# Kernel tuning notes

Hardware: AMD Instinct MI355X
Metric: run time of the kernel (lower is better)

Reference implementation:

```python
import jax, jax.numpy as jnp
import numpy as np

B, SQ, ST, SI = 8, 4096, 77, 16
C, DC, H = 1280, 2048, 20
DH = C // H  # 64
SCALE = 1.0 / np.sqrt(DH).astype(np.float32)
SCALE_ID = 1.0
SCALE_HAIR = 1.0


def setup_inputs() -> dict:
    key = jax.random.key(0)
    ks = jax.random.split(key, 12)
    std = 0.02
    return {
        "hidden_states": jax.random.normal(ks[0], (B, SQ, C), jnp.float32),
        "text_states": jax.random.normal(ks[1], (B, ST, DC), jnp.float32),
        "id_states": jax.random.normal(ks[2], (B, SI, DC), jnp.float32),
        "hair_states": jax.random.normal(ks[3], (B, SI, DC), jnp.float32),
        # weights stored as [in, out] (transpose of torch nn.Linear layout)
        "Wq": jax.random.normal(ks[4], (C, C), jnp.float32) * std,
        "Wk": jax.random.normal(ks[5], (DC, C), jnp.float32) * std,
        "Wv": jax.random.normal(ks[6], (DC, C), jnp.float32) * std,
        "Wo": jax.random.normal(ks[7], (C, C), jnp.float32) * std,
        "b_o": jnp.zeros((C,), jnp.float32),
        "Wk_id": jax.random.normal(ks[8], (DC, C), jnp.float32) * std,
        "Wv_id": jax.random.normal(ks[9], (DC, C), jnp.float32) * std,
        "Wk_hair": jax.random.normal(ks[10], (DC, C), jnp.float32) * std,
        "Wv_hair": jax.random.normal(ks[11], (DC, C), jnp.float32) * std,
    }


def _heads(x):
    # [B, S, C] -> [B, H, S, DH]
    b, s, _ = x.shape
    return x.reshape(b, s, H, DH).transpose(0, 2, 1, 3)


def _merge(x):
    # [B, H, S, DH] -> [B, S, C]
    b, h, s, d = x.shape
    return x.transpose(0, 2, 1, 3).reshape(b, s, h * d)


def _attend(q, k, v):
    # q: [B,H,Sq,DH], k/v: [B,H,Sk,DH]; fp32 scores (attn_fp32=True)
    scores = jnp.einsum("bhqd,bhkd->bhqk", q.astype(jnp.float32), k.astype(jnp.float32)) * SCALE
    p = jax.nn.softmax(scores, axis=-1)
    return jnp.einsum("bhqk,bhkd->bhqd", p, v.astype(jnp.float32))


def reference(hidden_states, text_states, id_states, hair_states, Wq, Wk, Wv, Wo, b_o, Wk_id, Wv_id, Wk_hair, Wv_hair):
    q = _heads(hidden_states @ Wq)
    # base cross-attention to text (standard diffusers AttnProcessor)
    base = _attend(q, _heads(text_states @ Wk), _heads(text_states @ Wv))
    result = _merge(base) @ Wo + b_o
    # ID branch: own K/V projections, shared query and to_out
    out_id = _attend(q, _heads(id_states @ Wk_id), _heads(id_states @ Wv_id))
    result = result + SCALE_ID * (_merge(out_id) @ Wo + b_o)
    # hair branch
    out_h = _attend(q, _heads(hair_states @ Wk_hair), _heads(hair_states @ Wv_hair))
    result = result + SCALE_HAIR * (_merge(out_h) @ Wo + b_o)
    return result
```

## Files before the change

kernel.cpp:

```cpp
#include <hip/hip_runtime.h>
#include <cstdint>
#include <cstddef>

typedef unsigned short u16;
typedef __attribute__((ext_vector_type(4))) float     f32x4_t;
typedef __attribute__((ext_vector_type(8))) __bf16    bf16x8_t;
typedef __attribute__((ext_vector_type(8))) u16       u16x8_t;
typedef __attribute__((ext_vector_type(4))) u16       u16x4_t;
typedef __attribute__((ext_vector_type(4))) float     fvec4_t;

#define DEVI __device__ __forceinline__

constexpr int Bn  = 8;
constexpr int SQn = 4096;
constexpr int STn = 77;
constexpr int SIn = 16;
constexpr int Cn  = 1280;
constexpr int DCn = 2048;
constexpr int Hn  = 20;
constexpr float SCALEf = 0.125f;
constexpr float L2E    = 1.4426950408889634f;

typedef const __attribute__((address_space(1))) void* gas_t;
typedef __attribute__((address_space(3))) void*       las_t;

DEVI u16 f2bf(float f) {
  union { float f; unsigned u; } cv; cv.f = f;
  unsigned u = cv.u;
  return (u16)((u + 0x7FFFu + ((u >> 16) & 1u)) >> 16);
}

__global__ __launch_bounds__(256) void cast_bf16_kernel(
    const float* __restrict__ src, u16* __restrict__ dst, int n8) {
  int i = blockIdx.x * 256 + threadIdx.x;
  if (i >= n8) return;
  const fvec4_t* s4 = (const fvec4_t*)src;
  fvec4_t a = s4[2 * i], b = s4[2 * i + 1];
  u16x8_t o;
  o[0] = f2bf(a[0]); o[1] = f2bf(a[1]); o[2] = f2bf(a[2]); o[3] = f2bf(a[3]);
  o[4] = f2bf(b[0]); o[5] = f2bf(b[1]); o[6] = f2bf(b[2]); o[7] = f2bf(b[3]);
  ((u16x8_t*)dst)[i] = o;
}

struct TrArgs {
  const float* src[8];
  u16*         dst[8];
  int          Kd[8];
};

__global__ __launch_bounds__(256) void transpose_cast_kernel(TrArgs ta) {
  int z = blockIdx.z;
  int K = ta.Kd[z];
  int k0 = blockIdx.x * 32;
  if (k0 >= K) return;
  int n0 = blockIdx.y * 32;
  __shared__ float tile[32][33];
  int tx = threadIdx.x & 31, ty = threadIdx.x >> 5;
  const float* src = ta.src[z];
#pragma unroll
  for (int i = 0; i < 4; i++) {
    int r = ty + 8 * i;
    tile[r][tx] = src[(size_t)(k0 + r) * Cn + n0 + tx];
  }
  __syncthreads();
  u16* dst = ta.dst[z];
#pragma unroll
  for (int i = 0; i < 4; i++) {
    int r = ty + 8 * i;
    dst[(size_t)(n0 + r) * K + k0 + tx] = f2bf(tile[tx][r]);
  }
}

template <int OUT_MODE, int A_HM>
__global__ __launch_bounds__(512, 2) void gemm256_kernel(
    const u16* __restrict__ A, const u16* __restrict__ Bt,
    void* __restrict__ Cout, const float* __restrict__ bias, int M, int K) {
  __shared__ __align__(16) u16 lds[2][2][256 * 64];
  const int t = threadIdx.x;
  const int w = t >> 6, l = t & 63;
  const int wr = w >> 2, wc = w & 3;
  const int lr = l & 15;
  const int m0 = blockIdx.x * 256, n0 = blockIdx.y * 256;
  const int NT = K >> 6;

  f32x4_t acc[8][4];
#pragma unroll
  for (int am = 0; am < 8; am++)
#pragma unroll
    for (int an = 0; an < 4; an++) {
      f32x4_t z = {0.f, 0.f, 0.f, 0.f};
      acc[am][an] = z;
    }

  auto stagePart = [&](int cb, int kt, int i) {
    const int k0 = kt * 64;
    int row = i * 64 + w * 8 + (l >> 3);
    int col16 = (l & 7) ^ (row & 7);
    const u16* ga;
    if (A_HM) {
      int gr = m0 + row, bb = gr >> 12, ss = gr & 4095;
      ga = A + (((size_t)bb * Hn + kt) * SQn + ss) * 64 + col16 * 8;
    } else {
      ga = A + (size_t)(m0 + row) * K + k0 + col16 * 8;
    }
    __builtin_amdgcn_global_load_lds((gas_t)ga, (las_t)(&lds[cb][0][0] + (size_t)(i * 512 + w * 64) * 8), 16, 0, 0);
    const u16* gb = Bt + (size_t)(n0 + row) * K + k0 + col16 * 8;
    __builtin_amdgcn_global_load_lds((gas_t)gb, (las_t)(&lds[cb][1][0] + (size_t)(i * 512 + w * 64) * 8), 16, 0, 0);
  };
  auto readA8 = [&](bf16x8_t (&dst)[8], const u16* bA, int kh) {
#pragma unroll
    for (int m = 0; m < 8; m++) {
      int row = wr * 128 + m * 16 + lr;
      int slot = kh * 4 + (l >> 4);
      dst[m] = *(const bf16x8_t*)&bA[row * 64 + ((slot ^ (row & 7)) * 8)];
    }
  };
  auto readB4 = [&](bf16x8_t (&dst)[4], const u16* bB, int kh) {
#pragma unroll
    for (int n = 0; n < 4; n++) {
      int row = wc * 64 + n * 16 + lr;
      int slot = kh * 4 + (l >> 4);
      dst[n] = *(const bf16x8_t*)&bB[row * 64 + ((slot ^ (row & 7)) * 8)];
    }
  };
  auto mfma32 = [&](bf16x8_t (&Af)[8], bf16x8_t (&Bf)[4]) {
    __builtin_amdgcn_s_setprio(1);
#pragma unroll
    for (int m = 0; m < 8; m++)
#pragma unroll
      for (int n = 0; n < 4; n++)
        acc[m][n] = __builtin_amdgcn_mfma_f32_16x16x32_bf16(Af[m], Bf[n], acc[m][n], 0, 0, 0);
    __builtin_amdgcn_s_setprio(0);
  };

#pragma unroll
  for (int i = 0; i < 4; i++) stagePart(0, 0, i);
#pragma unroll
  for (int i = 0; i < 4; i++) stagePart(1, 1, i);
  asm volatile("s_waitcnt vmcnt(8)" ::: "memory");
  __builtin_amdgcn_sched_barrier(0);
  __builtin_amdgcn_s_barrier();

  for (int kt = 0; kt < NT; kt++) {
    const int cb = kt & 1;
    const u16* bA = &lds[cb][0][0];
    const u16* bB = &lds[cb][1][0];
    const bool st = (kt + 2 < NT);
    bf16x8_t Af[8], Bf[4];

    readA8(Af, bA, 0);
    readB4(Bf, bB, 0);
    asm volatile("s_waitcnt lgkmcnt(0)" ::: "memory");
    __builtin_amdgcn_sched_barrier(0);
    mfma32(Af, Bf);

    readA8(Af, bA, 1);
    readB4(Bf, bB, 1);
    __builtin_amdgcn_s_barrier();
    if (st) {
      stagePart(cb, kt + 2, 0); stagePart(cb, kt + 2, 1);
      stagePart(cb, kt + 2, 2); stagePart(cb, kt + 2, 3);
    }
    asm volatile("s_waitcnt lgkmcnt(0)" ::: "memory");
    __builtin_amdgcn_sched_barrier(0);
    mfma32(Af, Bf);

    if (st) {
      asm volatile("s_waitcnt vmcnt(8)" ::: "memory");
    } else if (kt + 1 < NT) {
      asm volatile("s_waitcnt vmcnt(0)" ::: "memory");
    }
    __builtin_amdgcn_sched_barrier(0);
    __builtin_amdgcn_s_barrier();
  }

#pragma unroll
  for (int am = 0; am < 8; am++) {
    int rbase = m0 + wr * 128 + am * 16 + (l >> 4) * 4;
#pragma unroll
    for (int an = 0; an < 4; an++) {
      int col = n0 + wc * 64 + an * 16 + lr;
#pragma unroll
      for (int j = 0; j < 4; j++) {
        int r = rbase + j;
        if (OUT_MODE == 1) {
          ((float*)Cout)[(size_t)r * Cn + col] = acc[am][an][j] + 3.0f * bias[col];
        } else {
          int bb = r >> 12, ss = r & 4095;
          int hh = (n0 >> 6) + wc, dd = an * 16 + lr;
          ((u16*)Cout)[(((size_t)bb * Hn + hh) * SQn + ss) * 64 + dd] = f2bf(acc[am][an][j]);
        }
      }
    }
  }
}

DEVI void gemm_body(const u16* __restrict__ A, const u16* __restrict__ Bt,
                    u16* __restrict__ Cout, int M, int S, int K, int mtile, int ntile) {
  __shared__ __align__(16) u16 lA[128 * 64];
  __shared__ __align__(16) u16 lB[128 * 64];
  const int t = threadIdx.x;
  const int w = t >> 6, l = t & 63;
  const int wr = w >> 1, wc = w & 1;
  const int m0 = mtile * 128, n0 = ntile * 128;
  const int lr = l & 15, lk = (l >> 4) * 8;

  f32x4_t acc[4][4];
#pragma unroll
  for (int m = 0; m < 4; m++)
#pragma unroll
    for (int n = 0; n < 4; n++) {
      f32x4_t z = {0.f, 0.f, 0.f, 0.f};
      acc[m][n] = z;
    }

  for (int k0 = 0; k0 < K; k0 += 64) {
    __syncthreads();
#pragma unroll
    for (int i = 0; i < 4; i++) {
      int c = i * 256 + t;
      int row = c >> 3, ch = c & 7;
      int rA = m0 + row;
      rA = rA < M ? rA : M - 1;
      const u16* ga = A + (size_t)rA * K + k0 + ch * 8;
      __builtin_amdgcn_global_load_lds((gas_t)ga, (las_t)&lA[(i * 256 + w * 64) * 8], 16, 0, 0);
      const u16* gb = Bt + (size_t)(n0 + row) * K + k0 + ch * 8;
      __builtin_amdgcn_global_load_lds((gas_t)gb, (las_t)&lB[(i * 256 + w * 64) * 8], 16, 0, 0);
    }
    __syncthreads();
#pragma unroll
    for (int kk = 0; kk < 2; kk++) {
      bf16x8_t af[4], bf[4];
#pragma unroll
      for (int m = 0; m < 4; m++)
        af[m] = *(const bf16x8_t*)&lA[(64 * wr + 16 * m + lr) * 64 + kk * 32 + lk];
#pragma unroll
      for (int n = 0; n < 4; n++)
        bf[n] = *(const bf16x8_t*)&lB[(64 * wc + 16 * n + lr) * 64 + kk * 32 + lk];
#pragma unroll
      for (int m = 0; m < 4; m++)
#pragma unroll
        for (int n = 0; n < 4; n++)
          acc[m][n] = __builtin_amdgcn_mfma_f32_16x16x32_bf16(af[m], bf[n], acc[m][n], 0, 0, 0);
    }
  }

  const int rj = (l >> 4) * 4;
  const int hh = ntile * 2 + wc;
#pragma unroll
  for (int m = 0; m < 4; m++) {
    int rbase = m0 + 64 * wr + 16 * m + rj;
#pragma unroll
    for (int n = 0; n < 4; n++) {
      int dd = 16 * n + lr;
#pragma unroll
      for (int j = 0; j < 4; j++) {
        int r = rbase + j;
        if (r < M) {
          int bb = r / S, ss = r - bb * S;
          Cout[(((size_t)bb * Hn + hh) * S + ss) * 64 + dd] = f2bf(acc[m][n][j]);
        }
      }
    }
  }
}

struct KV6 {
  const u16* A[6];
  const u16* Bt[6];
  u16*       Cp[6];
  int        M[6];
  int        S[6];
};

__global__ __launch_bounds__(256) void gemm_kv_kernel(KV6 kv) {
  int z = blockIdx.z;
  int M = kv.M[z];
  if ((int)blockIdx.x * 128 >= M) return;
  gemm_body(kv.A[z], kv.Bt[z], kv.Cp[z], M, kv.S[z], DCn, blockIdx.x, blockIdx.y);
}

__global__ __launch_bounds__(256) void attn_kernel(
    const u16* __restrict__ q,
    const u16* __restrict__ ktx, const u16* __restrict__ vtx,
    const u16* __restrict__ kid, const u16* __restrict__ vid,
    const u16* __restrict__ kh,  const u16* __restrict__ vh,
    u16* __restrict__ osum) {
  __shared__ __align__(16) u16 KP[4 * 16 * 136];
  __shared__ __align__(16) u16 Vt[64 * 128];

  const int t = threadIdx.x, w = t >> 6, l = t & 63;
  const int bh = blockIdx.y;
  const int lr = l & 15, lk = (l >> 4) * 8;

  const u16* qB   = q   + ((size_t)bh) * SQn * 64;
  const u16* ktxB = ktx + ((size_t)bh) * STn * 64;
  const u16* vtxB = vtx + ((size_t)bh) * STn * 64;
  const u16* kidB = kid + ((size_t)bh) * SIn * 64;
  const u16* vidB = vid + ((size_t)bh) * SIn * 64;
  const u16* khB  = kh  + ((size_t)bh) * SIn * 64;
  const u16* vhB  = vh  + ((size_t)bh) * SIn * 64;
  u16*       oB   = osum + ((size_t)bh) * SQn * 64;

  for (int i = t; i < 112 * 8; i += 256) {
    int row = i >> 3, ch = i & 7;
    u16x8_t vv;
#pragma unroll
    for (int x = 0; x < 8; x++) vv[x] = 0;
    if (row < 77)
      vv = *(const u16x8_t*)(ktxB + (size_t)row * 64 + ch * 8);
    else if (row >= 80 && row < 96)
      vv = *(const u16x8_t*)(kidB + (size_t)(row - 80) * 64 + ch * 8);
    else if (row >= 96)
      vv = *(const u16x8_t*)(khB + (size_t)(row - 96) * 64 + ch * 8);
    *(u16x8_t*)&KP[row * 72 + ch * 8] = vv;
  }
  for (int i = t; i < 128 * 8; i += 256) {
    int key = i >> 3, ch = i & 7;
    u16x8_t vv;
#pragma unroll
    for (int x = 0; x < 8; x++) vv[x] = 0;
    if (key < 77)
      vv = *(const u16x8_t*)(vtxB + (size_t)key * 64 + ch * 8);
    else if (key >= 80 && key < 96)
      vv = *(const u16x8_t*)(vidB + (size_t)(key - 80) * 64 + ch * 8);
    else if (key >= 96 && key < 112)
      vv = *(const u16x8_t*)(vhB + (size_t)(key - 96) * 64 + ch * 8);
    int G = key >> 3, wk = key & 7;
#pragma unroll
    for (int x = 0; x < 8; x++) {
      int d = ch * 8 + x;
      int Gs = G ^ x ^ ch;
      Vt[d * 128 + Gs * 8 + wk] = vv[x];
    }
  }
  __syncthreads();

  bf16x8_t kf[7][2];
#pragma unroll
  for (int tt = 0; tt < 7; tt++)
#pragma unroll
    for (int kk = 0; kk < 2; kk++)
      kf[tt][kk] = *(const bf16x8_t*)&KP[(tt * 16 + lr) * 72 + kk * 32 + lk];
  __syncthreads();

  u16* Pw = &KP[w * 16 * 136];
  {
    u16x4_t z4; z4[0] = 0; z4[1] = 0; z4[2] = 0; z4[3] = 0;
    *(u16x4_t*)&Pw[(l >> 2) * 136 + 112 + (l & 3) * 4] = z4;
  }

  for (int rt = 0; rt < 8; rt++) {
    const int s0 = blockIdx.x * 512 + w * 128 + rt * 16;
    bf16x8_t qf[2];
#pragma unroll
    for (int kk = 0; kk < 2; kk++)
      qf[kk] = *(const bf16x8_t*)&qB[(size_t)(s0 + lr) * 64 + kk * 32 + lk];

    f32x4_t sc[7];
#pragma unroll
    for (int tt = 0; tt < 7; tt++) {
      f32x4_t z = {0.f, 0.f, 0.f, 0.f};
      z = __builtin_amdgcn_mfma_f32_16x16x32_bf16(qf[0], kf[tt][0], z, 0, 0, 0);
      z = __builtin_amdgcn_mfma_f32_16x16x32_bf16(qf[1], kf[tt][1], z, 0, 0, 0);
      sc[tt] = z;
    }
#pragma unroll
    for (int tt = 0; tt < 7; tt++)
#pragma unroll
      for (int j = 0; j < 4; j++) sc[tt][j] *= SCALEf;
    if (lr >= 13) {
#pragma unroll
      for (int j = 0; j < 4; j++) sc[4][j] = -3.0e38f;
    }

    float mx[4], sm[4], inv[4];

#pragma unroll
    for (int j = 0; j < 4; j++) {
      float m = sc[0][j];
      m = fmaxf(m, sc[1][j]); m = fmaxf(m, sc[2][j]);
      m = fmaxf(m, sc[3][j]); m = fmaxf(m, sc[4][j]);
      mx[j] = m;
    }
#pragma unroll
    for (int d = 1; d < 16; d <<= 1)
#pragma unroll
      for (int j = 0; j < 4; j++) mx[j] = fmaxf(mx[j], __shfl_xor(mx[j], d));
#pragma unroll
    for (int j = 0; j < 4; j++) sm[j] = 0.f;
#pragma unroll
    for (int tt = 0; tt < 5; tt++)
#pragma unroll
      for (int j = 0; j < 4; j++) {
        float p = __builtin_amdgcn_exp2f((sc[tt][j] - mx[j]) * L2E);
        sc[tt][j] = p;
        sm[j] += p;
      }
#pragma unroll
    for (int d = 1; d < 16; d <<= 1)
#pragma unroll
      for (int j = 0; j < 4; j++) sm[j] += __shfl_xor(sm[j], d);
#pragma unroll
    for (int j = 0; j < 4; j++) inv[j] = __builtin_amdgcn_rcpf(sm[j]);
#pragma unroll
    for (int tt = 0; tt < 5; tt++)
#pragma unroll
      for (int j = 0; j < 4; j++) {
        __bf16 pb = (__bf16)(sc[tt][j] * inv[j]);
        Pw[((l >> 4) * 4 + j) * 136 + tt * 16 + lr] = *(u16*)&pb;
      }

#pragma unroll
    for (int j = 0; j < 4; j++) mx[j] = sc[5][j];
#pragma unroll
    for (int d = 1; d < 16; d <<= 1)
#pragma unroll
      for (int j = 0; j < 4; j++) mx[j] = fmaxf(mx[j], __shfl_xor(mx[j], d));
#pragma unroll
    for (int j = 0; j < 4; j++) {
      float p = __builtin_amdgcn_exp2f((sc[5][j] - mx[j]) * L2E);
      sc[5][j] = p;
      sm[j] = p;
    }
#pragma unroll
    for (int d = 1; d < 16; d <<= 1)
#pragma unroll
      for (int j = 0; j < 4; j++) sm[j] += __shfl_xor(sm[j], d);
#pragma unroll
    for (int j = 0; j < 4; j++) {
      __bf16 pb = (__bf16)(sc[5][j] * __builtin_amdgcn_rcpf(sm[j]));
      Pw[((l >> 4) * 4 + j) * 136 + 80 + lr] = *(u16*)&pb;
    }

#pragma unroll
    for (int j = 0; j < 4; j++) mx[j] = sc[6][j];
#pragma unroll
    for (int d = 1; d < 16; d <<= 1)
#pragma unroll
      for (int j = 0; j < 4; j++) mx[j] = fmaxf(mx[j], __shfl_xor(mx[j], d));
#pragma unroll
    for (int j = 0; j < 4; j++) {
      float p = __builtin_amdgcn_exp2f((sc[6][j] - mx[j]) * L2E);
      sc[6][j] = p;
      sm[j] = p;
    }
#pragma unroll
    for (int d = 1; d < 16; d <<= 1)
#pragma unroll
      for (int j = 0; j < 4; j++) sm[j] += __shfl_xor(sm[j], d);
#pragma unroll
    for (int j = 0; j < 4; j++) {
      __bf16 pb = (__bf16)(sc[6][j] * __builtin_amdgcn_rcpf(sm[j]));
      Pw[((l >> 4) * 4 + j) * 136 + 96 + lr] = *(u16*)&pb;
    }

    f32x4_t oacc[4];
#pragma unroll
    for (int n = 0; n < 4; n++) {
      f32x4_t z = {0.f, 0.f, 0.f, 0.f};
      oacc[n] = z;
    }
#pragma unroll
    for (int ktile = 0; ktile < 4; ktile++) {
      bf16x8_t pf = *(const bf16x8_t*)&Pw[lr * 136 + ktile * 32 + lk];
#pragma unroll
      for (int n = 0; n < 4; n++) {
        int d = 16 * n + lr;
        int Gs = (4 * ktile + (l >> 4)) ^ (d & 7) ^ ((d >> 3) & 7);
        bf16x8_t vf = *(const bf16x8_t*)&Vt[d * 128 + Gs * 8];
        oacc[n] = __builtin_amdgcn_mfma_f32_16x16x32_bf16(pf, vf, oacc[n], 0, 0, 0);
      }
    }
#pragma unroll
    for (int n = 0; n < 4; n++)
#pragma unroll
      for (int j = 0; j < 4; j++) {
        int srow = s0 + (l >> 4) * 4 + j;
        __bf16 ob = (__bf16)oacc[n][j];
        oB[(size_t)srow * 64 + 16 * n + lr] = *(u16*)&ob;
      }
  }
}

extern "C" void kernel_launch(void* const* d_in, const int* in_sizes, int n_in,
                              void* d_out, int out_size, void* d_ws, size_t ws_size,
                              hipStream_t stream) {
  (void)in_sizes; (void)n_in; (void)out_size; (void)ws_size;
  const float* hidden  = (const float*)d_in[0];
  const float* text    = (const float*)d_in[1];
  const float* ids     = (const float*)d_in[2];
  const float* hair    = (const float*)d_in[3];
  const float* Wq      = (const float*)d_in[4];
  const float* Wk      = (const float*)d_in[5];
  const float* Wv      = (const float*)d_in[6];
  const float* Wo      = (const float*)d_in[7];
  const float* b_o     = (const float*)d_in[8];
  const float* Wk_id   = (const float*)d_in[9];
  const float* Wv_id   = (const float*)d_in[10];
  const float* Wk_hair = (const float*)d_in[11];
  const float* Wv_hair = (const float*)d_in[12];
  float* out = (float*)d_out;

  char* ws = (char*)d_ws;
  size_t off = 0;
  auto carve = [&](size_t bytes) -> char* {
    char* p = ws + off;
    off += (bytes + 255) & ~(size_t)255;
    return p;
  };

  u16* h_bf    = (u16*)carve((size_t)Bn * SQn * Cn * 2);
  u16* q_bf    = (u16*)carve((size_t)Bn * SQn * Cn * 2);
  u16* text_bf = (u16*)carve((size_t)Bn * STn * DCn * 2);
  u16* id_bf   = (u16*)carve((size_t)Bn * SIn * DCn * 2);
  u16* hair_bf = (u16*)carve((size_t)Bn * SIn * DCn * 2);
  u16* Wq_t    = (u16*)carve((size_t)Cn * Cn * 2);
  u16* Wo_t    = (u16*)carve((size_t)Cn * Cn * 2);
  u16* Wk_t    = (u16*)carve((size_t)DCn * Cn * 2);
  u16* Wv_t    = (u16*)carve((size_t)DCn * Cn * 2);
  u16* Wkid_t  = (u16*)carve((size_t)DCn * Cn * 2);
  u16* Wvid_t  = (u16*)carve((size_t)DCn * Cn * 2);
  u16* Wkh_t   = (u16*)carve((size_t)DCn * Cn * 2);
  u16* Wvh_t   = (u16*)carve((size_t)DCn * Cn * 2);
  u16* k_text  = (u16*)carve((size_t)Bn * STn * Cn * 2);
  u16* v_text  = (u16*)carve((size_t)Bn * STn * Cn * 2);
  u16* k_id    = (u16*)carve((size_t)Bn * SIn * Cn * 2);
  u16* v_id    = (u16*)carve((size_t)Bn * SIn * Cn * 2);
  u16* k_hr    = (u16*)carve((size_t)Bn * SIn * Cn * 2);
  u16* v_hr    = (u16*)carve((size_t)Bn * SIn * Cn * 2);
  u16* attn_sum = h_bf;

  {
    int n8 = Bn * SQn * Cn / 8;
    cast_bf16_kernel<<<dim3((n8 + 255) / 256), 256, 0, stream>>>(hidden, h_bf, n8);
  }
  {
    int n8 = Bn * STn * DCn / 8;
    cast_bf16_kernel<<<dim3((n8 + 255) / 256), 256, 0, stream>>>(text, text_bf, n8);
  }
  {
    int n8 = Bn * SIn * DCn / 8;
    cast_bf16_kernel<<<dim3((n8 + 255) / 256), 256, 0, stream>>>(ids, id_bf, n8);
    cast_bf16_kernel<<<dim3((n8 + 255) / 256), 256, 0, stream>>>(hair, hair_bf, n8);
  }

  {
    TrArgs ta;
    ta.src[0] = Wq;      ta.dst[0] = Wq_t;   ta.Kd[0] = Cn;
    ta.src[1] = Wo;      ta.dst[1] = Wo_t;   ta.Kd[1] = Cn;
    ta.src[2] = Wk;      ta.dst[2] = Wk_t;   ta.Kd[2] = DCn;
    ta.src[3] = Wv;      ta.dst[3] = Wv_t;   ta.Kd[3] = DCn;
    ta.src[4] = Wk_id;   ta.dst[4] = Wkid_t; ta.Kd[4] = DCn;
    ta.src[5] = Wv_id;   ta.dst[5] = Wvid_t; ta.Kd[5] = DCn;
    ta.src[6] = Wk_hair; ta.dst[6] = Wkh_t;  ta.Kd[6] = DCn;
    ta.src[7] = Wv_hair; ta.dst[7] = Wvh_t;  ta.Kd[7] = DCn;
    transpose_cast_kernel<<<dim3(DCn / 32, Cn / 32, 8), 256, 0, stream>>>(ta);
  }

  gemm256_kernel<2, 0><<<dim3(Bn * SQn / 256, Cn / 256), 512, 0, stream>>>(
      h_bf, Wq_t, q_bf, nullptr, Bn * SQn, Cn);

  {
    KV6 kv;
    kv.A[0] = text_bf; kv.Bt[0] = Wk_t;   kv.Cp[0] = k_text; kv.M[0] = Bn * STn; kv.S[0] = STn;
    kv.A[1] = text_bf; kv.Bt[1] = Wv_t;   kv.Cp[1] = v_text; kv.M[1] = Bn * STn; kv.S[1] = STn;
    kv.A[2] = id_bf;   kv.Bt[2] = Wkid_t; kv.Cp[2] = k_id;   kv.M[2] = Bn * SIn; kv.S[2] = SIn;
    kv.A[3] = id_bf;   kv.Bt[3] = Wvid_t; kv.Cp[3] = v_id;   kv.M[3] = Bn * SIn; kv.S[3] = SIn;
    kv.A[4] = hair_bf; kv.Bt[4] = Wkh_t;  kv.Cp[4] = k_hr;   kv.M[4] = Bn * SIn; kv.S[4] = SIn;
    kv.A[5] = hair_bf; kv.Bt[5] = Wvh_t;  kv.Cp[5] = v_hr;   kv.M[5] = Bn * SIn; kv.S[5] = SIn;
    gemm_kv_kernel<<<dim3((Bn * STn + 127) / 128, Cn / 128, 6), 256, 0, stream>>>(kv);
  }

  attn_kernel<<<dim3(SQn / 512, Bn * Hn), 256, 0, stream>>>(
      q_bf, k_text, v_text, k_id, v_id, k_hr, v_hr, attn_sum);

  gemm256_kernel<1, 1><<<dim3(Bn * SQn / 256, Cn / 256), 512, 0, stream>>>(
      attn_sum, Wo_t, out, b_o, Bn * SQn, Cn);
}
```

Baseline: 475.5 us.

## Merge input casts into one launch and co-schedule Q and KV projections

The four separate fp32-to-bf16 cast launches become one kernel that picks its source and destination from the flat thread index. The Q projection GEMM and the six small K/V projection GEMMs now share a single launch: the first 640 blocks compute 256x256 Q tiles, and the remaining 70 blocks each run two 128x128 K/V tiles, one per 256-thread half. This removes launch gaps and lets the small K/V work fill the tail of the Q GEMM. The cost is a shared 128KB LDS allocation for the K/V blocks, and both halves of a block must keep their barriers in lockstep, which holds because they run the same K loop.

```diff
diff --git a/kernel.cpp b/kernel.cpp
--- a/kernel.cpp
+++ b/kernel.cpp
@@ -21,6 +21,12 @@
 constexpr float SCALEf = 0.125f;
 constexpr float L2E    = 1.4426950408889634f;
 
+constexpr int CAST_N0 = Bn * SQn * Cn / 8;
+constexpr int CAST_N1 = Bn * STn * DCn / 8;
+constexpr int CAST_N2 = Bn * SIn * DCn / 8;
+constexpr int CAST_N3 = Bn * SIn * DCn / 8;
+constexpr int CAST_NT = CAST_N0 + CAST_N1 + CAST_N2 + CAST_N3;
+
 typedef const __attribute__((address_space(1))) void* gas_t;
 typedef __attribute__((address_space(3))) void*       las_t;
 
@@ -30,16 +36,23 @@
   return (u16)((u + 0x7FFFu + ((u >> 16) & 1u)) >> 16);
 }
 
-__global__ __launch_bounds__(256) void cast_bf16_kernel(
-    const float* __restrict__ src, u16* __restrict__ dst, int n8) {
+__global__ __launch_bounds__(256) void cast4_kernel(
+    const float* __restrict__ hs, const float* __restrict__ tx,
+    const float* __restrict__ idp, const float* __restrict__ hrp,
+    u16* __restrict__ dh, u16* __restrict__ dt,
+    u16* __restrict__ di, u16* __restrict__ dr) {
   int i = blockIdx.x * 256 + threadIdx.x;
-  if (i >= n8) return;
+  const float* src; u16* dst; int off;
+  if (i < CAST_N0)                              { src = hs;  dst = dh; off = i; }
+  else if (i < CAST_N0 + CAST_N1)               { src = tx;  dst = dt; off = i - CAST_N0; }
+  else if (i < CAST_N0 + CAST_N1 + CAST_N2)     { src = idp; dst = di; off = i - CAST_N0 - CAST_N1; }
+  else                                          { src = hrp; dst = dr; off = i - CAST_N0 - CAST_N1 - CAST_N2; }
   const fvec4_t* s4 = (const fvec4_t*)src;
-  fvec4_t a = s4[2 * i], b = s4[2 * i + 1];
+  fvec4_t a = s4[2 * off], b = s4[2 * off + 1];
   u16x8_t o;
   o[0] = f2bf(a[0]); o[1] = f2bf(a[1]); o[2] = f2bf(a[2]); o[3] = f2bf(a[3]);
   o[4] = f2bf(b[0]); o[5] = f2bf(b[1]); o[6] = f2bf(b[2]); o[7] = f2bf(b[3]);
-  ((u16x8_t*)dst)[i] = o;
+  ((u16x8_t*)dst)[off] = o;
 }
 
 struct TrArgs {
@@ -72,15 +85,15 @@
 }
 
 template <int OUT_MODE, int A_HM>
-__global__ __launch_bounds__(512, 2) void gemm256_kernel(
-    const u16* __restrict__ A, const u16* __restrict__ Bt,
-    void* __restrict__ Cout, const float* __restrict__ bias, int M, int K) {
-  __shared__ __align__(16) u16 lds[2][2][256 * 64];
+DEVI void gemm256_body(u16* sm, const u16* __restrict__ A,
+                       const u16* __restrict__ Bt, void* __restrict__ Cout,
+                       const float* __restrict__ bias, int M, int K,
+                       int mtile, int ntile) {
   const int t = threadIdx.x;
   const int w = t >> 6, l = t & 63;
   const int wr = w >> 2, wc = w & 3;
   const int lr = l & 15;
-  const int m0 = blockIdx.x * 256, n0 = blockIdx.y * 256;
+  const int m0 = mtile * 256, n0 = ntile * 256;
   const int NT = K >> 6;
 
   f32x4_t acc[8][4];
@@ -103,9 +116,9 @@
     } else {
       ga = A + (size_t)(m0 + row) * K + k0 + col16 * 8;
     }
-    __builtin_amdgcn_global_load_lds((gas_t)ga, (las_t)(&lds[cb][0][0] + (size_t)(i * 512 + w * 64) * 8), 16, 0, 0);
+    __builtin_amdgcn_global_load_lds((gas_t)ga, (las_t)(sm + (size_t)(cb * 2 + 0) * 16384 + (size_t)(i * 512 + w * 64) * 8), 16, 0, 0);
     const u16* gb = Bt + (size_t)(n0 + row) * K + k0 + col16 * 8;
-    __builtin_amdgcn_global_load_lds((gas_t)gb, (las_t)(&lds[cb][1][0] + (size_t)(i * 512 + w * 64) * 8), 16, 0, 0);
+    __builtin_amdgcn_global_load_lds((gas_t)gb, (las_t)(sm + (size_t)(cb * 2 + 1) * 16384 + (size_t)(i * 512 + w * 64) * 8), 16, 0, 0);
   };
   auto readA8 = [&](bf16x8_t (&dst)[8], const u16* bA, int kh) {
 #pragma unroll
@@ -143,8 +156,8 @@
 
   for (int kt = 0; kt < NT; kt++) {
     const int cb = kt & 1;
-    const u16* bA = &lds[cb][0][0];
-    const u16* bB = &lds[cb][1][0];
+    const u16* bA = sm + (size_t)(cb * 2 + 0) * 16384;
+    const u16* bB = sm + (size_t)(cb * 2 + 1) * 16384;
     const bool st = (kt + 2 < NT);
     bf16x8_t Af[8], Bf[4];
 
@@ -195,12 +208,12 @@
   }
 }
 
-DEVI void gemm_body(const u16* __restrict__ A, const u16* __restrict__ Bt,
-                    u16* __restrict__ Cout, int M, int S, int K, int mtile, int ntile) {
-  __shared__ __align__(16) u16 lA[128 * 64];
-  __shared__ __align__(16) u16 lB[128 * 64];
-  const int t = threadIdx.x;
-  const int w = t >> 6, l = t & 63;
+DEVI void kv_body(u16* lsA, int th, const u16* __restrict__ A,
+                  const u16* __restrict__ Bt, u16* __restrict__ Cout,
+                  int M, int S, int mtile, int ntile) {
+  u16* lA = lsA;
+  u16* lB = lsA + 8192;
+  const int w = th >> 6, l = th & 63;
   const int wr = w >> 1, wc = w & 1;
   const int m0 = mtile * 128, n0 = ntile * 128;
   const int lr = l & 15, lk = (l >> 4) * 8;
@@ -214,17 +227,17 @@
       acc[m][n] = z;
     }
 
-  for (int k0 = 0; k0 < K; k0 += 64) {
+  for (int k0 = 0; k0 < DCn; k0 += 64) {
     __syncthreads();
 #pragma unroll
     for (int i = 0; i < 4; i++) {
-      int c = i * 256 + t;
+      int c = i * 256 + th;
       int row = c >> 3, ch = c & 7;
       int rA = m0 + row;
       rA = rA < M ? rA : M - 1;
-      const u16* ga = A + (size_t)rA * K + k0 + ch * 8;
+      const u16* ga = A + (size_t)rA * DCn + k0 + ch * 8;
       __builtin_amdgcn_global_load_lds((gas_t)ga, (las_t)&lA[(i * 256 + w * 64) * 8], 16, 0, 0);
-      const u16* gb = Bt + (size_t)(n0 + row) * K + k0 + ch * 8;
+      const u16* gb = Bt + (size_t)(n0 + row) * DCn + k0 + ch * 8;
       __builtin_amdgcn_global_load_lds((gas_t)gb, (las_t)&lB[(i * 256 + w * 64) * 8], 16, 0, 0);
     }
     __syncthreads();
@@ -265,19 +278,34 @@
   }
 }
 
-struct KV6 {
-  const u16* A[6];
-  const u16* Bt[6];
-  u16*       Cp[6];
-  int        M[6];
-  int        S[6];
+struct QKVArgs {
+  const u16* hq;  const u16* WqT;  u16* qout;
+  const u16* A[6]; const u16* Bt[6]; u16* Cp[6]; int M[6]; int S[6];
 };
 
-__global__ __launch_bounds__(256) void gemm_kv_kernel(KV6 kv) {
-  int z = blockIdx.z;
-  int M = kv.M[z];
-  if ((int)blockIdx.x * 128 >= M) return;
-  gemm_body(kv.A[z], kv.Bt[z], kv.Cp[z], M, kv.S[z], DCn, blockIdx.x, blockIdx.y);
+__global__ __launch_bounds__(512, 2) void gemm_q_kv_kernel(QKVArgs a) {
+  __shared__ __align__(16) u16 sm[65536];
+  const int bx = blockIdx.x;
+  if (bx < 640) {
+    gemm256_body<2, 0>(sm, a.hq, a.WqT, a.qout, nullptr,
+                       Bn * SQn, Cn, bx % 128, bx / 128);
+  } else {
+    const int p = bx - 640;
+    const int h = threadIdx.x >> 8;
+    const int kt = p * 2 + h;
+    int z, mt, nt;
+    if (kt < 100) { z = kt / 50; int r = kt % 50; mt = r / 10; nt = r % 10; }
+    else          { int r = kt - 100; z = 2 + r / 10; mt = 0; nt = r % 10; }
+    kv_body(sm + (size_t)h * 16384, threadIdx.x & 255,
+            a.A[z], a.Bt[z], a.Cp[z], a.M[z], a.S[z], mt, nt);
+  }
+}
+
+__global__ __launch_bounds__(512, 2) void gemm_o_kernel(
+    const u16* __restrict__ A, const u16* __restrict__ Bt,
+    float* __restrict__ Cout, const float* __restrict__ bias, int M, int K) {
+  __shared__ __align__(16) u16 sm[65536];
+  gemm256_body<1, 1>(sm, A, Bt, Cout, bias, M, K, blockIdx.x, blockIdx.y);
 }
 
 __global__ __launch_bounds__(256) void attn_kernel(
@@ -531,19 +559,8 @@
   u16* v_hr    = (u16*)carve((size_t)Bn * SIn * Cn * 2);
   u16* attn_sum = h_bf;
 
-  {
-    int n8 = Bn * SQn * Cn / 8;
-    cast_bf16_kernel<<<dim3((n8 + 255) / 256), 256, 0, stream>>>(hidden, h_bf, n8);
-  }
-  {
-    int n8 = Bn * STn * DCn / 8;
-    cast_bf16_kernel<<<dim3((n8 + 255) / 256), 256, 0, stream>>>(text, text_bf, n8);
-  }
-  {
-    int n8 = Bn * SIn * DCn / 8;
-    cast_bf16_kernel<<<dim3((n8 + 255) / 256), 256, 0, stream>>>(ids, id_bf, n8);
-    cast_bf16_kernel<<<dim3((n8 + 255) / 256), 256, 0, stream>>>(hair, hair_bf, n8);
-  }
+  cast4_kernel<<<dim3(CAST_NT / 256), 256, 0, stream>>>(
+      hidden, text, ids, hair, h_bf, text_bf, id_bf, hair_bf);
 
   {
     TrArgs ta;
@@ -558,23 +575,21 @@
     transpose_cast_kernel<<<dim3(DCn / 32, Cn / 32, 8), 256, 0, stream>>>(ta);
   }
 
-  gemm256_kernel<2, 0><<<dim3(Bn * SQn / 256, Cn / 256), 512, 0, stream>>>(
-      h_bf, Wq_t, q_bf, nullptr, Bn * SQn, Cn);
-
   {
-    KV6 kv;
-    kv.A[0] = text_bf; kv.Bt[0] = Wk_t;   kv.Cp[0] = k_text; kv.M[0] = Bn * STn; kv.S[0] = STn;
-    kv.A[1] = text_bf; kv.Bt[1] = Wv_t;   kv.Cp[1] = v_text; kv.M[1] = Bn * STn; kv.S[1] = STn;
-    kv.A[2] = id_bf;   kv.Bt[2] = Wkid_t; kv.Cp[2] = k_id;   kv.M[2] = Bn * SIn; kv.S[2] = SIn;
-    kv.A[3] = id_bf;   kv.Bt[3] = Wvid_t; kv.Cp[3] = v_id;   kv.M[3] = Bn * SIn; kv.S[3] = SIn;
-    kv.A[4] = hair_bf; kv.Bt[4] = Wkh_t;  kv.Cp[4] = k_hr;   kv.M[4] = Bn * SIn; kv.S[4] = SIn;
-    kv.A[5] = hair_bf; kv.Bt[5] = Wvh_t;  kv.Cp[5] = v_hr;   kv.M[5] = Bn * SIn; kv.S[5] = SIn;
-    gemm_kv_kernel<<<dim3((Bn * STn + 127) / 128, Cn / 128, 6), 256, 0, stream>>>(kv);
+    QKVArgs a;
+    a.hq = h_bf; a.WqT = Wq_t; a.qout = q_bf;
+    a.A[0] = text_bf; a.Bt[0] = Wk_t;   a.Cp[0] = k_text; a.M[0] = Bn * STn; a.S[0] = STn;
+    a.A[1] = text_bf; a.Bt[1] = Wv_t;   a.Cp[1] = v_text; a.M[1] = Bn * STn; a.S[1] = STn;
+    a.A[2] = id_bf;   a.Bt[2] = Wkid_t; a.Cp[2] = k_id;   a.M[2] = Bn * SIn; a.S[2] = SIn;
+    a.A[3] = id_bf;   a.Bt[3] = Wvid_t; a.Cp[3] = v_id;   a.M[3] = Bn * SIn; a.S[3] = SIn;
+    a.A[4] = hair_bf; a.Bt[4] = Wkh_t;  a.Cp[4] = k_hr;   a.M[4] = Bn * SIn; a.S[4] = SIn;
+    a.A[5] = hair_bf; a.Bt[5] = Wvh_t;  a.Cp[5] = v_hr;   a.M[5] = Bn * SIn; a.S[5] = SIn;
+    gemm_q_kv_kernel<<<dim3(710), 512, 0, stream>>>(a);
   }
 
   attn_kernel<<<dim3(SQn / 512, Bn * Hn), 256, 0, stream>>>(
       q_bf, k_text, v_text, k_id, v_id, k_hr, v_hr, attn_sum);
 
-  gemm256_kernel<1, 1><<<dim3(Bn * SQn / 256, Cn / 256), 512, 0, stream>>>(
+  gemm_o_kernel<<<dim3(Bn * SQn / 256, Cn / 256), 512, 0, stream>>>(
       attn_sum, Wo_t, out, b_o, Bn * SQn, Cn);
 }
```

New measurement: 459.3 us. 3.4% less time.
